# Performance work log

Measured on AMD Instinct MI355X. Metric: run time of the kernel, lower is better.

## Reference

```python
import jax, jax.numpy as jnp
import numpy as np

S, T, BERT, POS = 256, 512, 768, 128
H1 = 1024
NUM_CLASSES = 6


def setup_inputs() -> dict:
    key = jax.random.key(0)
    ks = jax.random.split(key, 12)
    emb = jax.random.normal(ks[0], (S, T, BERT), dtype=jnp.float32)
    pos = jax.random.normal(ks[1], (S, T, POS), dtype=jnp.float32)
    seg = jnp.sort(jax.random.randint(ks[2], (S,), 0, 64)).astype(jnp.int32)
    scale = 0.02
    return {
        "embeddings": emb,
        "position_encodings": pos,
        "W_attn": jax.random.normal(ks[3], (BERT + POS, 1), dtype=jnp.float32) * scale,
        "b_attn": jnp.zeros((1,), dtype=jnp.float32),
        "W1": jax.random.normal(ks[4], (BERT, H1), dtype=jnp.float32) * scale,
        "b1": jnp.zeros((H1,), dtype=jnp.float32),
        "W2": jax.random.normal(ks[5], (H1, H1), dtype=jnp.float32) * scale,
        "b2": jnp.zeros((H1,), dtype=jnp.float32),
        "W3": jax.random.normal(ks[6], (H1, NUM_CLASSES), dtype=jnp.float32) * scale,
        "b3": jnp.zeros((NUM_CLASSES,), dtype=jnp.float32),
        "segment_ids": seg,
        "num_comments": 64,
    }


def reference(embeddings, position_encodings, W_attn, b_attn, W1, b1, W2, b2, W3, b3, segment_ids, num_comments):
    # attention logits: Linear(bert+pos -> 1) over concatenated features, shape (S, T, 1)
    attn = jnp.concatenate([embeddings, position_encodings], axis=2) @ W_attn + b_attn
    # per-segment softmax over the 512-token dim (torch Softmax(1) on (b-a, 512, 1))
    w = jax.nn.softmax(attn, axis=1)
    # softmax-weighted pooling per segment -> (S, BERT)
    segvec = jnp.sum(w * embeddings, axis=1)
    # ragged sum over each comment's segments (contiguous bounds == sorted segment ids)
    vecs = jax.ops.segment_sum(segvec, segment_ids, num_segments=num_comments)
    # MLP head with LeakyReLU (torch default slope 0.01) and Sigmoid
    h = jax.nn.leaky_relu(vecs @ W1 + b1, negative_slope=0.01)
    h = jax.nn.leaky_relu(h @ W2 + b2, negative_slope=0.01)
    return jax.nn.sigmoid(h @ W3 + b3)
```

## Files before the change

### kernel.cpp

```cpp
#include <hip/hip_runtime.h>
#include <math.h>
#include <stdint.h>

#define S_SEQ 256
#define T_TOK 512
#define BERT 768
#define POSD 128
#define H1 1024
#define NC 6

#define CHUNK_T 128
#define WTOK 32

__device__ __forceinline__ float wave_sum64(float x) {
    x += __int_as_float(__builtin_amdgcn_update_dpp(
            0, __float_as_int(x), 0x128, 0xF, 0xF, true));
    x += __int_as_float(__builtin_amdgcn_update_dpp(
            0, __float_as_int(x), 0x124, 0xF, 0xF, true));
    x += __int_as_float(__builtin_amdgcn_update_dpp(
            0, __float_as_int(x), 0x122, 0xF, 0xF, true));
    x += __int_as_float(__builtin_amdgcn_update_dpp(
            0, __float_as_int(x), 0x121, 0xF, 0xF, true));
    float a = x, b = x;
    asm("v_permlane16_swap_b32 %0, %1" : "+v"(a), "+v"(b));
    x = a + b;
    a = x; b = x;
    asm("v_permlane32_swap_b32 %0, %1" : "+v"(a), "+v"(b));
    return a + b;
}

__global__ __launch_bounds__(256, 4) void pool_kernel(
    const float* __restrict__ emb, const float* __restrict__ pos,
    const float* __restrict__ Wa, const float* __restrict__ ba,
    float* __restrict__ part_acc, float* __restrict__ part_ml)
{
    __shared__ float mg[4 * BERT];
    __shared__ float wml[8];

    const int tid = threadIdx.x;
    const int w   = tid >> 6;
    const int l   = tid & 63;
    const int b   = blockIdx.x;
    const int s   = b >> 2;
    const int t0  = (b & 3) * CHUNK_T + w * WTOK;

    const float4* Wa4 = (const float4*)Wa;
    const float4 wa0 = Wa4[l];
    const float4 wa1 = Wa4[64 + l];
    const float4 wa2 = Wa4[128 + l];
    const float2 wp  = ((const float2*)(Wa + BERT))[l];
    const float  bav = ba[0];

    const float4* erow = (const float4*)(emb + ((size_t)s * T_TOK + t0) * BERT);
    const float2* prow = (const float2*)(pos + ((size_t)s * T_TOK + t0) * POSD);

    float m = -INFINITY, lsum = 0.f;
    float acc[12];
    #pragma unroll
    for (int j = 0; j < 12; ++j) acc[j] = 0.f;

    float4 na0 = erow[l],       na1 = erow[64 + l],  na2 = erow[128 + l];
    float4 nb0 = erow[192 + l], nb1 = erow[256 + l], nb2 = erow[320 + l];
    float2 nq0 = prow[l],       nq1 = prow[64 + l];

    for (int i = 0; i < WTOK; i += 2) {
        const float4 a0 = na0, a1 = na1, a2 = na2;
        const float4 b0 = nb0, b1 = nb1, b2 = nb2;
        const float2 q0 = nq0, q1 = nq1;

        if (i + 2 < WTOK) {
            const float4* rn = erow + (size_t)(i + 2) * (BERT / 4);
            na0 = rn[l];       na1 = rn[64 + l];  na2 = rn[128 + l];
            nb0 = rn[192 + l]; nb1 = rn[256 + l]; nb2 = rn[320 + l];
            nq0 = prow[(i + 2) * (POSD / 2) + l];
            nq1 = prow[(i + 3) * (POSD / 2) + l];
        }

        float d0 = a0.x*wa0.x + a0.y*wa0.y + a0.z*wa0.z + a0.w*wa0.w
                 + a1.x*wa1.x + a1.y*wa1.y + a1.z*wa1.z + a1.w*wa1.w
                 + a2.x*wa2.x + a2.y*wa2.y + a2.z*wa2.z + a2.w*wa2.w
                 + q0.x*wp.x  + q0.y*wp.y;
        float d1 = b0.x*wa0.x + b0.y*wa0.y + b0.z*wa0.z + b0.w*wa0.w
                 + b1.x*wa1.x + b1.y*wa1.y + b1.z*wa1.z + b1.w*wa1.w
                 + b2.x*wa2.x + b2.y*wa2.y + b2.z*wa2.z + b2.w*wa2.w
                 + q1.x*wp.x  + q1.y*wp.y;

        d0 = wave_sum64(d0);
        d1 = wave_sum64(d1);

        const float lg0 = d0 + bav;
        const float lg1 = d1 + bav;
        const float mn  = fmaxf(m, fmaxf(lg0, lg1));
        const float alpha = __expf(m - mn);
        const float p0 = __expf(lg0 - mn);
        const float p1 = __expf(lg1 - mn);
        lsum = lsum * alpha + p0 + p1;
        m = mn;

        acc[0]  = fmaf(p0, a0.x, fmaf(p1, b0.x, acc[0]  * alpha));
        acc[1]  = fmaf(p0, a0.y, fmaf(p1, b0.y, acc[1]  * alpha));
        acc[2]  = fmaf(p0, a0.z, fmaf(p1, b0.z, acc[2]  * alpha));
        acc[3]  = fmaf(p0, a0.w, fmaf(p1, b0.w, acc[3]  * alpha));
        acc[4]  = fmaf(p0, a1.x, fmaf(p1, b1.x, acc[4]  * alpha));
        acc[5]  = fmaf(p0, a1.y, fmaf(p1, b1.y, acc[5]  * alpha));
        acc[6]  = fmaf(p0, a1.z, fmaf(p1, b1.z, acc[6]  * alpha));
        acc[7]  = fmaf(p0, a1.w, fmaf(p1, b1.w, acc[7]  * alpha));
        acc[8]  = fmaf(p0, a2.x, fmaf(p1, b2.x, acc[8]  * alpha));
        acc[9]  = fmaf(p0, a2.y, fmaf(p1, b2.y, acc[9]  * alpha));
        acc[10] = fmaf(p0, a2.z, fmaf(p1, b2.z, acc[10] * alpha));
        acc[11] = fmaf(p0, a2.w, fmaf(p1, b2.w, acc[11] * alpha));
    }

    #pragma unroll
    for (int j = 0; j < 4; ++j) {
        mg[w * BERT +       l * 4 + j] = acc[j];
        mg[w * BERT + 256 + l * 4 + j] = acc[4 + j];
        mg[w * BERT + 512 + l * 4 + j] = acc[8 + j];
    }
    if (l == 0) { wml[w * 2] = m; wml[w * 2 + 1] = lsum; }
    __syncthreads();

    const float m0 = wml[0], l0 = wml[1], m1 = wml[2], l1 = wml[3];
    const float m2 = wml[4], l2 = wml[5], m3 = wml[6], l3 = wml[7];
    const float M  = fmaxf(fmaxf(m0, m1), fmaxf(m2, m3));
    const float e0 = __expf(m0 - M), e1 = __expf(m1 - M);
    const float e2 = __expf(m2 - M), e3 = __expf(m3 - M);
    const float lt = l0 * e0 + l1 * e1 + l2 * e2 + l3 * e3;
    #pragma unroll
    for (int k = 0; k < 3; ++k) {
        const int col = tid * 3 + k;
        part_acc[(size_t)b * BERT + col] =
              e0 * mg[col] + e1 * mg[BERT + col]
            + e2 * mg[2 * BERT + col] + e3 * mg[3 * BERT + col];
    }
    if (tid == 0) { part_ml[b * 2] = M; part_ml[b * 2 + 1] = lt; }
}

__global__ void combine_segsum(
    const float* __restrict__ part_acc, const float* __restrict__ part_ml,
    const int* __restrict__ seg, float* __restrict__ vecs,
    const float* __restrict__ b1, const float* __restrict__ b2,
    float* __restrict__ h1, float* __restrict__ h2)
{
    const int c = blockIdx.x;
    const int tid = threadIdx.x;

    for (int j = tid; j < H1; j += 256) {
        h1[(size_t)c * H1 + j] = b1[j];
        h2[(size_t)c * H1 + j] = b2[j];
    }

    float v0 = 0.f, v1 = 0.f, v2 = 0.f;
    for (int s = 0; s < S_SEQ; ++s) {
        if (seg[s] != c) continue;
        const int p = s * 4;
        const float m0 = part_ml[(p+0)*2], l0 = part_ml[(p+0)*2+1];
        const float m1 = part_ml[(p+1)*2], l1 = part_ml[(p+1)*2+1];
        const float m2 = part_ml[(p+2)*2], l2 = part_ml[(p+2)*2+1];
        const float m3 = part_ml[(p+3)*2], l3 = part_ml[(p+3)*2+1];
        const float M  = fmaxf(fmaxf(m0, m1), fmaxf(m2, m3));
        const float e0 = __expf(m0 - M), e1 = __expf(m1 - M);
        const float e2 = __expf(m2 - M), e3 = __expf(m3 - M);
        const float inv = 1.0f / (l0*e0 + l1*e1 + l2*e2 + l3*e3);
        const int col = tid * 3;
        v0 += inv * (e0 * part_acc[(size_t)(p+0)*BERT + col]
                   + e1 * part_acc[(size_t)(p+1)*BERT + col]
                   + e2 * part_acc[(size_t)(p+2)*BERT + col]
                   + e3 * part_acc[(size_t)(p+3)*BERT + col]);
        v1 += inv * (e0 * part_acc[(size_t)(p+0)*BERT + col + 1]
                   + e1 * part_acc[(size_t)(p+1)*BERT + col + 1]
                   + e2 * part_acc[(size_t)(p+2)*BERT + col + 1]
                   + e3 * part_acc[(size_t)(p+3)*BERT + col + 1]);
        v2 += inv * (e0 * part_acc[(size_t)(p+0)*BERT + col + 2]
                   + e1 * part_acc[(size_t)(p+1)*BERT + col + 2]
                   + e2 * part_acc[(size_t)(p+2)*BERT + col + 2]
                   + e3 * part_acc[(size_t)(p+3)*BERT + col + 2]);
    }
    vecs[(size_t)c*BERT + tid*3 + 0] = v0;
    vecs[(size_t)c*BERT + tid*3 + 1] = v1;
    vecs[(size_t)c*BERT + tid*3 + 2] = v2;
}

__global__ __launch_bounds__(256) void mlp_layer_part(
    const float* __restrict__ in, const float* __restrict__ W,
    float* __restrict__ out, int K, int lr_in)
{
    __shared__ float v[256];
    const int c      = blockIdx.y;
    const int kchunk = K >> 2;
    const int k0     = blockIdx.z * kchunk;
    const int tid    = threadIdx.x;
    const int j      = blockIdx.x * 256 + tid;

    if (tid < kchunk) {
        float x = in[(size_t)c * K + k0 + tid];
        if (lr_in) x = x > 0.f ? x : 0.01f * x;
        v[tid] = x;
    }
    __syncthreads();

    float a0 = 0.f, a1 = 0.f, a2 = 0.f, a3 = 0.f;
    const float* Wp = W + (size_t)k0 * H1 + j;
    #pragma unroll 4
    for (int k = 0; k < kchunk; k += 4) {
        a0 = fmaf(v[k    ], Wp[(size_t)(k    ) * H1], a0);
        a1 = fmaf(v[k + 1], Wp[(size_t)(k + 1) * H1], a1);
        a2 = fmaf(v[k + 2], Wp[(size_t)(k + 2) * H1], a2);
        a3 = fmaf(v[k + 3], Wp[(size_t)(k + 3) * H1], a3);
    }
    atomicAdd(&out[(size_t)c * H1 + j], (a0 + a1) + (a2 + a3));
}

__global__ void mlp_out(
    const float* __restrict__ h, const float* __restrict__ W3,
    const float* __restrict__ b3, float* __restrict__ out)
{
    __shared__ float v[H1];
    __shared__ float red[NC][4];
    const int c = blockIdx.x;
    const int tid = threadIdx.x;
    const int wave = tid >> 6, lane = tid & 63;
    for (int i = tid; i < H1; i += 256) {
        float x = h[(size_t)c * H1 + i];
        v[i] = x > 0.f ? x : 0.01f * x;
    }
    __syncthreads();
    float po[NC] = {0.f, 0.f, 0.f, 0.f, 0.f, 0.f};
    for (int k = tid; k < H1; k += 256) {
        const float hv = v[k];
        #pragma unroll
        for (int o = 0; o < NC; ++o) po[o] = fmaf(hv, W3[k * NC + o], po[o]);
    }
    #pragma unroll
    for (int o = 0; o < NC; ++o) {
        float d = po[o];
        #pragma unroll
        for (int off = 32; off >= 1; off >>= 1) d += __shfl_xor(d, off, 64);
        if (lane == 0) red[o][wave] = d;
    }
    __syncthreads();
    if (tid < NC) {
        const float sum = red[tid][0] + red[tid][1] + red[tid][2] + red[tid][3] + b3[tid];
        out[c * NC + tid] = 1.0f / (1.0f + __expf(-sum));
    }
}

extern "C" void kernel_launch(void* const* d_in, const int* in_sizes, int n_in,
                              void* d_out, int out_size, void* d_ws, size_t ws_size,
                              hipStream_t stream)
{
    const float* emb = (const float*)d_in[0];
    const float* pos = (const float*)d_in[1];
    const float* Wa  = (const float*)d_in[2];
    const float* ba  = (const float*)d_in[3];
    const float* W1  = (const float*)d_in[4];
    const float* b1  = (const float*)d_in[5];
    const float* W2  = (const float*)d_in[6];
    const float* b2  = (const float*)d_in[7];
    const float* W3  = (const float*)d_in[8];
    const float* b3  = (const float*)d_in[9];
    const int*   seg = (const int*)d_in[10];
    float* out = (float*)d_out;

    float* ws = (float*)d_ws;
    float* part_acc = ws;
    float* part_ml  = part_acc + 1024 * BERT;
    float* vecs     = part_ml  + 1024 * 2;
    float* h1       = vecs     + 64 * BERT;
    float* h2       = h1       + 64 * H1;

    pool_kernel<<<1024, 256, 0, stream>>>(emb, pos, Wa, ba, part_acc, part_ml);
    combine_segsum<<<64, 256, 0, stream>>>(part_acc, part_ml, seg, vecs,
                                           b1, b2, h1, h2);
    mlp_layer_part<<<dim3(4, 64, 4), 256, 0, stream>>>(vecs, W1, h1, BERT, 0);
    mlp_layer_part<<<dim3(4, 64, 4), 256, 0, stream>>>(h1, W2, h2, H1, 1);
    mlp_out<<<64, 256, 0, stream>>>(h2, W3, b3, out);
}
```

Baseline: 629.8 us.

## Reuse MLP weights across comments, skip redundant softmax rescales, coalesce partials

The MLP layer kernel now processes four comments per block, so each weight load feeds four accumulators, and it splits K eight ways. The online softmax skips the alpha rescale when the running max does not increase. Partial-accumulator columns use a strided layout for coalesced stores and loads. Bias initialisation of the hidden buffers moves into the pooling kernel, which removes that work from the combine kernel. The trade-off is more atomics per block and a branch in the hot loop.

```diff
diff --git a/kernel.cpp b/kernel.cpp
--- a/kernel.cpp
+++ b/kernel.cpp
@@ -11,6 +11,9 @@
 
 #define CHUNK_T 128
 #define WTOK 32
+
+#define CPB 4
+#define KSPLIT 8
 
 __device__ __forceinline__ float wave_sum64(float x) {
     x += __int_as_float(__builtin_amdgcn_update_dpp(
@@ -32,7 +35,9 @@
 __global__ __launch_bounds__(256, 4) void pool_kernel(
     const float* __restrict__ emb, const float* __restrict__ pos,
     const float* __restrict__ Wa, const float* __restrict__ ba,
-    float* __restrict__ part_acc, float* __restrict__ part_ml)
+    float* __restrict__ part_acc, float* __restrict__ part_ml,
+    const float* __restrict__ b1, const float* __restrict__ b2,
+    float* __restrict__ h1, float* __restrict__ h2)
 {
     __shared__ float mg[4 * BERT];
     __shared__ float wml[8];
@@ -51,6 +56,14 @@
     const float2 wp  = ((const float2*)(Wa + BERT))[l];
     const float  bav = ba[0];
 
+    if (b < 64) {
+        #pragma unroll
+        for (int j = tid; j < H1; j += 256) {
+            h1[(size_t)b * H1 + j] = b1[j];
+            h2[(size_t)b * H1 + j] = b2[j];
+        }
+    }
+
     const float4* erow = (const float4*)(emb + ((size_t)s * T_TOK + t0) * BERT);
     const float2* prow = (const float2*)(pos + ((size_t)s * T_TOK + t0) * POSD);
 
@@ -65,7 +78,7 @@
 
     for (int i = 0; i < WTOK; i += 2) {
         const float4 a0 = na0, a1 = na1, a2 = na2;
-        const float4 b0 = nb0, b1 = nb1, b2 = nb2;
+        const float4 b0 = nb0, b1v = nb1, b2v = nb2;
         const float2 q0 = nq0, q1 = nq1;
 
         if (i + 2 < WTOK) {
@@ -81,8 +94,8 @@
                  + a2.x*wa2.x + a2.y*wa2.y + a2.z*wa2.z + a2.w*wa2.w
                  + q0.x*wp.x  + q0.y*wp.y;
         float d1 = b0.x*wa0.x + b0.y*wa0.y + b0.z*wa0.z + b0.w*wa0.w
-                 + b1.x*wa1.x + b1.y*wa1.y + b1.z*wa1.z + b1.w*wa1.w
-                 + b2.x*wa2.x + b2.y*wa2.y + b2.z*wa2.z + b2.w*wa2.w
+                 + b1v.x*wa1.x + b1v.y*wa1.y + b1v.z*wa1.z + b1v.w*wa1.w
+                 + b2v.x*wa2.x + b2v.y*wa2.y + b2v.z*wa2.z + b2v.w*wa2.w
                  + q1.x*wp.x  + q1.y*wp.y;
 
         d0 = wave_sum64(d0);
@@ -90,25 +103,43 @@
 
         const float lg0 = d0 + bav;
         const float lg1 = d1 + bav;
-        const float mn  = fmaxf(m, fmaxf(lg0, lg1));
-        const float alpha = __expf(m - mn);
-        const float p0 = __expf(lg0 - mn);
-        const float p1 = __expf(lg1 - mn);
-        lsum = lsum * alpha + p0 + p1;
-        m = mn;
-
-        acc[0]  = fmaf(p0, a0.x, fmaf(p1, b0.x, acc[0]  * alpha));
-        acc[1]  = fmaf(p0, a0.y, fmaf(p1, b0.y, acc[1]  * alpha));
-        acc[2]  = fmaf(p0, a0.z, fmaf(p1, b0.z, acc[2]  * alpha));
-        acc[3]  = fmaf(p0, a0.w, fmaf(p1, b0.w, acc[3]  * alpha));
-        acc[4]  = fmaf(p0, a1.x, fmaf(p1, b1.x, acc[4]  * alpha));
-        acc[5]  = fmaf(p0, a1.y, fmaf(p1, b1.y, acc[5]  * alpha));
-        acc[6]  = fmaf(p0, a1.z, fmaf(p1, b1.z, acc[6]  * alpha));
-        acc[7]  = fmaf(p0, a1.w, fmaf(p1, b1.w, acc[7]  * alpha));
-        acc[8]  = fmaf(p0, a2.x, fmaf(p1, b2.x, acc[8]  * alpha));
-        acc[9]  = fmaf(p0, a2.y, fmaf(p1, b2.y, acc[9]  * alpha));
-        acc[10] = fmaf(p0, a2.z, fmaf(p1, b2.z, acc[10] * alpha));
-        acc[11] = fmaf(p0, a2.w, fmaf(p1, b2.w, acc[11] * alpha));
+        const float mx  = fmaxf(lg0, lg1);
+
+        if (mx > m) {
+            const float alpha = __expf(m - mx);
+            const float p0 = __expf(lg0 - mx);
+            const float p1 = __expf(lg1 - mx);
+            lsum = lsum * alpha + p0 + p1;
+            m = mx;
+            acc[0]  = fmaf(p0, a0.x, fmaf(p1, b0.x, acc[0]  * alpha));
+            acc[1]  = fmaf(p0, a0.y, fmaf(p1, b0.y, acc[1]  * alpha));
+            acc[2]  = fmaf(p0, a0.z, fmaf(p1, b0.z, acc[2]  * alpha));
+            acc[3]  = fmaf(p0, a0.w, fmaf(p1, b0.w, acc[3]  * alpha));
+            acc[4]  = fmaf(p0, a1.x, fmaf(p1, b1v.x, acc[4]  * alpha));
+            acc[5]  = fmaf(p0, a1.y, fmaf(p1, b1v.y, acc[5]  * alpha));
+            acc[6]  = fmaf(p0, a1.z, fmaf(p1, b1v.z, acc[6]  * alpha));
+            acc[7]  = fmaf(p0, a1.w, fmaf(p1, b1v.w, acc[7]  * alpha));
+            acc[8]  = fmaf(p0, a2.x, fmaf(p1, b2v.x, acc[8]  * alpha));
+            acc[9]  = fmaf(p0, a2.y, fmaf(p1, b2v.y, acc[9]  * alpha));
+            acc[10] = fmaf(p0, a2.z, fmaf(p1, b2v.z, acc[10] * alpha));
+            acc[11] = fmaf(p0, a2.w, fmaf(p1, b2v.w, acc[11] * alpha));
+        } else {
+            const float p0 = __expf(lg0 - m);
+            const float p1 = __expf(lg1 - m);
+            lsum += p0 + p1;
+            acc[0]  = fmaf(p0, a0.x, fmaf(p1, b0.x, acc[0]));
+            acc[1]  = fmaf(p0, a0.y, fmaf(p1, b0.y, acc[1]));
+            acc[2]  = fmaf(p0, a0.z, fmaf(p1, b0.z, acc[2]));
+            acc[3]  = fmaf(p0, a0.w, fmaf(p1, b0.w, acc[3]));
+            acc[4]  = fmaf(p0, a1.x, fmaf(p1, b1v.x, acc[4]));
+            acc[5]  = fmaf(p0, a1.y, fmaf(p1, b1v.y, acc[5]));
+            acc[6]  = fmaf(p0, a1.z, fmaf(p1, b1v.z, acc[6]));
+            acc[7]  = fmaf(p0, a1.w, fmaf(p1, b1v.w, acc[7]));
+            acc[8]  = fmaf(p0, a2.x, fmaf(p1, b2v.x, acc[8]));
+            acc[9]  = fmaf(p0, a2.y, fmaf(p1, b2v.y, acc[9]));
+            acc[10] = fmaf(p0, a2.z, fmaf(p1, b2v.z, acc[10]));
+            acc[11] = fmaf(p0, a2.w, fmaf(p1, b2v.w, acc[11]));
+        }
     }
 
     #pragma unroll
@@ -128,7 +159,7 @@
     const float lt = l0 * e0 + l1 * e1 + l2 * e2 + l3 * e3;
     #pragma unroll
     for (int k = 0; k < 3; ++k) {
-        const int col = tid * 3 + k;
+        const int col = tid + 256 * k;
         part_acc[(size_t)b * BERT + col] =
               e0 * mg[col] + e1 * mg[BERT + col]
             + e2 * mg[2 * BERT + col] + e3 * mg[3 * BERT + col];
@@ -138,18 +169,10 @@
 
 __global__ void combine_segsum(
     const float* __restrict__ part_acc, const float* __restrict__ part_ml,
-    const int* __restrict__ seg, float* __restrict__ vecs,
-    const float* __restrict__ b1, const float* __restrict__ b2,
-    float* __restrict__ h1, float* __restrict__ h2)
+    const int* __restrict__ seg, float* __restrict__ vecs)
 {
     const int c = blockIdx.x;
     const int tid = threadIdx.x;
-
-    for (int j = tid; j < H1; j += 256) {
-        h1[(size_t)c * H1 + j] = b1[j];
-        h2[(size_t)c * H1 + j] = b2[j];
-    }
-
     float v0 = 0.f, v1 = 0.f, v2 = 0.f;
     for (int s = 0; s < S_SEQ; ++s) {
         if (seg[s] != c) continue;
@@ -162,53 +185,59 @@
         const float e0 = __expf(m0 - M), e1 = __expf(m1 - M);
         const float e2 = __expf(m2 - M), e3 = __expf(m3 - M);
         const float inv = 1.0f / (l0*e0 + l1*e1 + l2*e2 + l3*e3);
-        const int col = tid * 3;
-        v0 += inv * (e0 * part_acc[(size_t)(p+0)*BERT + col]
-                   + e1 * part_acc[(size_t)(p+1)*BERT + col]
-                   + e2 * part_acc[(size_t)(p+2)*BERT + col]
-                   + e3 * part_acc[(size_t)(p+3)*BERT + col]);
-        v1 += inv * (e0 * part_acc[(size_t)(p+0)*BERT + col + 1]
-                   + e1 * part_acc[(size_t)(p+1)*BERT + col + 1]
-                   + e2 * part_acc[(size_t)(p+2)*BERT + col + 1]
-                   + e3 * part_acc[(size_t)(p+3)*BERT + col + 1]);
-        v2 += inv * (e0 * part_acc[(size_t)(p+0)*BERT + col + 2]
-                   + e1 * part_acc[(size_t)(p+1)*BERT + col + 2]
-                   + e2 * part_acc[(size_t)(p+2)*BERT + col + 2]
-                   + e3 * part_acc[(size_t)(p+3)*BERT + col + 2]);
-    }
-    vecs[(size_t)c*BERT + tid*3 + 0] = v0;
-    vecs[(size_t)c*BERT + tid*3 + 1] = v1;
-    vecs[(size_t)c*BERT + tid*3 + 2] = v2;
+        v0 += inv * (e0 * part_acc[(size_t)(p+0)*BERT + tid]
+                   + e1 * part_acc[(size_t)(p+1)*BERT + tid]
+                   + e2 * part_acc[(size_t)(p+2)*BERT + tid]
+                   + e3 * part_acc[(size_t)(p+3)*BERT + tid]);
+        v1 += inv * (e0 * part_acc[(size_t)(p+0)*BERT + tid + 256]
+                   + e1 * part_acc[(size_t)(p+1)*BERT + tid + 256]
+                   + e2 * part_acc[(size_t)(p+2)*BERT + tid + 256]
+                   + e3 * part_acc[(size_t)(p+3)*BERT + tid + 256]);
+        v2 += inv * (e0 * part_acc[(size_t)(p+0)*BERT + tid + 512]
+                   + e1 * part_acc[(size_t)(p+1)*BERT + tid + 512]
+                   + e2 * part_acc[(size_t)(p+2)*BERT + tid + 512]
+                   + e3 * part_acc[(size_t)(p+3)*BERT + tid + 512]);
+    }
+    vecs[(size_t)c*BERT + tid      ] = v0;
+    vecs[(size_t)c*BERT + tid + 256] = v1;
+    vecs[(size_t)c*BERT + tid + 512] = v2;
 }
 
 __global__ __launch_bounds__(256) void mlp_layer_part(
     const float* __restrict__ in, const float* __restrict__ W,
     float* __restrict__ out, int K, int lr_in)
 {
-    __shared__ float v[256];
-    const int c      = blockIdx.y;
-    const int kchunk = K >> 2;
+    __shared__ float v[CPB][H1 / KSPLIT];
+    const int kchunk = K >> 3;
     const int k0     = blockIdx.z * kchunk;
+    const int c0     = blockIdx.y * CPB;
     const int tid    = threadIdx.x;
     const int j      = blockIdx.x * 256 + tid;
 
-    if (tid < kchunk) {
-        float x = in[(size_t)c * K + k0 + tid];
-        if (lr_in) x = x > 0.f ? x : 0.01f * x;
-        v[tid] = x;
+    #pragma unroll
+    for (int ci = 0; ci < CPB; ++ci) {
+        if (tid < kchunk) {
+            float x = in[(size_t)(c0 + ci) * K + k0 + tid];
+            if (lr_in) x = x > 0.f ? x : 0.01f * x;
+            v[ci][tid] = x;
+        }
     }
     __syncthreads();
 
     float a0 = 0.f, a1 = 0.f, a2 = 0.f, a3 = 0.f;
     const float* Wp = W + (size_t)k0 * H1 + j;
     #pragma unroll 4
-    for (int k = 0; k < kchunk; k += 4) {
-        a0 = fmaf(v[k    ], Wp[(size_t)(k    ) * H1], a0);
-        a1 = fmaf(v[k + 1], Wp[(size_t)(k + 1) * H1], a1);
-        a2 = fmaf(v[k + 2], Wp[(size_t)(k + 2) * H1], a2);
-        a3 = fmaf(v[k + 3], Wp[(size_t)(k + 3) * H1], a3);
-    }
-    atomicAdd(&out[(size_t)c * H1 + j], (a0 + a1) + (a2 + a3));
+    for (int k = 0; k < kchunk; ++k) {
+        const float wv = Wp[(size_t)k * H1];
+        a0 = fmaf(v[0][k], wv, a0);
+        a1 = fmaf(v[1][k], wv, a1);
+        a2 = fmaf(v[2][k], wv, a2);
+        a3 = fmaf(v[3][k], wv, a3);
+    }
+    atomicAdd(&out[(size_t)(c0 + 0) * H1 + j], a0);
+    atomicAdd(&out[(size_t)(c0 + 1) * H1 + j], a1);
+    atomicAdd(&out[(size_t)(c0 + 2) * H1 + j], a2);
+    atomicAdd(&out[(size_t)(c0 + 3) * H1 + j], a3);
 }
 
 __global__ void mlp_out(
@@ -269,10 +298,10 @@
     float* h1       = vecs     + 64 * BERT;
     float* h2       = h1       + 64 * H1;
 
-    pool_kernel<<<1024, 256, 0, stream>>>(emb, pos, Wa, ba, part_acc, part_ml);
-    combine_segsum<<<64, 256, 0, stream>>>(part_acc, part_ml, seg, vecs,
-                                           b1, b2, h1, h2);
-    mlp_layer_part<<<dim3(4, 64, 4), 256, 0, stream>>>(vecs, W1, h1, BERT, 0);
-    mlp_layer_part<<<dim3(4, 64, 4), 256, 0, stream>>>(h1, W2, h2, H1, 1);
+    pool_kernel<<<1024, 256, 0, stream>>>(emb, pos, Wa, ba, part_acc, part_ml,
+                                          b1, b2, h1, h2);
+    combine_segsum<<<64, 256, 0, stream>>>(part_acc, part_ml, seg, vecs);
+    mlp_layer_part<<<dim3(4, 16, 8), 256, 0, stream>>>(vecs, W1, h1, BERT, 0);
+    mlp_layer_part<<<dim3(4, 16, 8), 256, 0, stream>>>(h1, W2, h2, H1, 1);
     mlp_out<<<64, 256, 0, stream>>>(h2, W3, b3, out);
 }
```

Measured after the change: 630.3 us. Within noise of the previous version (+0.1%).
